# Kernel tuning notes

Measured on AMD Instinct MI355X. Metric: run time of the kernel, lower is better.

The kernel has to match this reference:

```python
import jax, jax.numpy as jnp
import numpy as np

N = 100_000   # num nodes (embedding_shape[0])
E = 1_600_000 # directed edges in adj_t
Q = 500_000   # query edges
D = 256       # embedding_dim == hidden_dim == output_dim


def setup_inputs() -> dict:
    key = jax.random.key(0)
    ks = jax.random.split(key, 12)
    adj_row = jax.random.randint(ks[0], (E,), 0, N, dtype=jnp.int64 if jax.config.jax_enable_x64 else jnp.int32)
    adj_col = jax.random.randint(ks[1], (E,), 0, N, dtype=adj_row.dtype)
    edges = jax.random.randint(ks[2], (2, Q), 0, N, dtype=adj_row.dtype)
    s = 1.0 / np.sqrt(D)
    emb = jax.random.normal(ks[3], (N, D), jnp.float32) * 0.02  # xavier-ish init
    W0 = jax.random.normal(ks[4], (D, D), jnp.float32) * s
    W1 = jax.random.normal(ks[5], (D, D), jnp.float32) * s
    W2 = jax.random.normal(ks[6], (D, D), jnp.float32) * s
    b0 = jnp.zeros((D,), jnp.float32)
    b1 = jnp.zeros((D,), jnp.float32)
    b2 = jnp.zeros((D,), jnp.float32)
    # LinkPredictor: 3 lins (D->D, D->D, D->1)
    P0 = jax.random.normal(ks[7], (D, D), jnp.float32) * s
    P1 = jax.random.normal(ks[8], (D, D), jnp.float32) * s
    P2 = jax.random.normal(ks[9], (D, 1), jnp.float32) * s
    pb0 = jnp.zeros((D,), jnp.float32)
    pb1 = jnp.zeros((D,), jnp.float32)
    pb2 = jnp.zeros((1,), jnp.float32)
    return dict(adj_row=adj_row, adj_col=adj_col, edges=edges, emb=emb,
                W0=W0, b0=b0, W1=W1, b1=b1, W2=W2, b2=b2,
                P0=P0, pb0=pb0, P1=P1, pb1=pb1, P2=P2, pb2=pb2)


def _gcn_norm(adj_row, adj_col):
    # add self loops, symmetric normalization D^-1/2 (A+I) D^-1/2
    loops = jnp.arange(N, dtype=adj_row.dtype)
    row = jnp.concatenate([adj_row, loops])
    col = jnp.concatenate([adj_col, loops])
    deg = jax.ops.segment_sum(jnp.ones(row.shape, jnp.float32), row, num_segments=N)
    dinv = jnp.where(deg > 0, jax.lax.rsqrt(jnp.maximum(deg, 1.0)), 0.0)
    norm = dinv[row] * dinv[col]  # [E+N]
    return row, col, norm


def _gcn_conv(x, W, b, row, col, norm):
    h = x @ W                                   # dense transform [N,D]
    msg = h[col] * norm[:, None]                # gather + scale [E+N,D]
    return jax.ops.segment_sum(msg, row, num_segments=N) + b


def reference(adj_row, adj_col, edges, emb,
              W0, b0, W1, b1, W2, b2,
              P0, pb0, P1, pb1, P2, pb2):
    row, col, norm = _gcn_norm(adj_row, adj_col)
    x = emb
    x = jax.nn.relu(_gcn_conv(x, W0, b0, row, col, norm))  # dropout: no-op (eval)
    x = jax.nn.relu(_gcn_conv(x, W1, b1, row, col, norm))
    x = _gcn_conv(x, W2, b2, row, col, norm)
    # edge-gather + LinkPredictor MLP
    h = x[edges[0]] * x[edges[1]]                # [Q,D]
    h = jax.nn.relu(h @ P0 + pb0)
    h = jax.nn.relu(h @ P1 + pb1)
    out = jax.nn.sigmoid(h @ P2 + pb2)           # [Q,1]
    return out[:, 0]
```

## Files before the change

### kernel.cpp

```cpp
#include <hip/hip_runtime.h>
#include <math.h>

#define D 256

typedef short short8 __attribute__((ext_vector_type(8)));
typedef float f32x4 __attribute__((ext_vector_type(4)));
typedef float f32x2 __attribute__((ext_vector_type(2)));

__device__ __forceinline__ float bf2f(unsigned int h) {
  return __uint_as_float(h << 16);
}
__device__ __forceinline__ unsigned short f2bf(float f) {
  unsigned int u = __float_as_uint(f);
  u += 0x7fffu + ((u >> 16) & 1u);
  return (unsigned short)(u >> 16);
}
__device__ __forceinline__ unsigned int packtrunc(float a, float b) {
  return (__float_as_uint(a) >> 16) | (__float_as_uint(b) & 0xffff0000u);
}
__device__ __forceinline__ unsigned int pk_fp8x4(float a, float b, float c, float d) {
  unsigned int r = 0;
  r = __builtin_amdgcn_cvt_pk_fp8_f32(a, b, r, false);
  r = __builtin_amdgcn_cvt_pk_fp8_f32(c, d, r, true);
  return r;
}
__device__ __forceinline__ void up_fp8x4(unsigned int x, float& a, float& b, float& c,
                                         float& d) {
  f32x2 lo = __builtin_amdgcn_cvt_pk_f32_fp8(x, false);
  f32x2 hi = __builtin_amdgcn_cvt_pk_f32_fp8(x, true);
  a = lo.x; b = lo.y; c = hi.x; d = hi.y;
}

__global__ __launch_bounds__(256) void k_count(const int* __restrict__ row,
                                               int* __restrict__ cnt, int E) {
  int i = blockIdx.x * 256 + threadIdx.x;
  if (i < E) atomicAdd(&cnt[row[i]], 1);
}

__global__ __launch_bounds__(256) void k_scan1(const int* __restrict__ cnt,
                                               int* __restrict__ bsum) {
  __shared__ int sw[4];
  int b = blockIdx.x, tid = threadIdx.x, lane = tid & 63, w = tid >> 6;
  int4 v = *(const int4*)(cnt + (size_t)b * 1024 + tid * 4);
  int s = v.x + v.y + v.z + v.w;
#pragma unroll
  for (int d = 32; d; d >>= 1) s += __shfl_xor(s, d, 64);
  if (lane == 0) sw[w] = s;
  __syncthreads();
  if (tid == 0) bsum[b] = sw[0] + sw[1] + sw[2] + sw[3];
}

__global__ __launch_bounds__(256) void k_scan2(int* __restrict__ bsum, int nb,
                                               int* __restrict__ offs_end) {
  __shared__ int sw[4];
  int tid = threadIdx.x, lane = tid & 63, w = tid >> 6;
  int v = (tid < nb) ? bsum[tid] : 0;
  int x = v;
#pragma unroll
  for (int d = 1; d < 64; d <<= 1) {
    int y = __shfl_up(x, d, 64);
    if (lane >= d) x += y;
  }
  if (lane == 63) sw[w] = x;
  __syncthreads();
  int woff = 0;
  for (int i = 0; i < w; ++i) woff += sw[i];
  int incl = woff + x;
  if (tid < nb) bsum[tid] = incl - v;
  if (tid == 0) *offs_end = sw[0] + sw[1] + sw[2] + sw[3];
}

__global__ __launch_bounds__(256) void k_scan3(const int* __restrict__ cnt,
                                               const int* __restrict__ bbase,
                                               int* __restrict__ offs,
                                               float* __restrict__ dinv) {
  __shared__ int sw[4];
  int b = blockIdx.x, tid = threadIdx.x, lane = tid & 63, w = tid >> 6;
  size_t base = (size_t)b * 1024 + tid * 4;
  int4 v = *(const int4*)(cnt + base);
  int s = v.x + v.y + v.z + v.w;
  int x = s;
#pragma unroll
  for (int d = 1; d < 64; d <<= 1) {
    int y = __shfl_up(x, d, 64);
    if (lane >= d) x += y;
  }
  if (lane == 63) sw[w] = x;
  __syncthreads();
  int woff = bbase[b];
  for (int i = 0; i < w; ++i) woff += sw[i];
  int excl = woff + x - s;
  int4 o;
  o.x = excl;
  o.y = excl + v.x;
  o.z = o.y + v.y;
  o.w = o.z + v.z;
  *(int4*)(offs + base) = o;
  float4 dv;
  dv.x = rsqrtf((float)(v.x + 1));
  dv.y = rsqrtf((float)(v.y + 1));
  dv.z = rsqrtf((float)(v.z + 1));
  dv.w = rsqrtf((float)(v.w + 1));
  *(float4*)(dinv + base) = dv;
}

__global__ __launch_bounds__(256) void k_scatter(const int* __restrict__ row,
                                                 const int* __restrict__ col,
                                                 const int* __restrict__ offs,
                                                 int* __restrict__ cursor,
                                                 const float* __restrict__ dinv,
                                                 int2* __restrict__ csr, int E) {
  int i = blockIdx.x * 256 + threadIdx.x;
  if (i >= E) return;
  int r = row[i];
  int c = col[i];
  int p = atomicAdd(&cursor[r], 1);
  int o = offs[r] + p;
  int2 cn;
  cn.x = c;
  cn.y = __float_as_int(dinv[r] * dinv[c]);
  csr[o] = cn;
}

__global__ __launch_bounds__(256) void k_cast_w(const float* __restrict__ W0,
                                                const float* __restrict__ W1,
                                                const float* __restrict__ W2,
                                                const float* __restrict__ P0,
                                                const float* __restrict__ P1,
                                                unsigned short* __restrict__ Wt) {
  int idx = blockIdx.x * 256 + threadIdx.x;
  int m = idx >> 16;
  int e = idx & 65535;
  int k = e >> 8;
  int n = e & 255;
  const float* src = (m == 0) ? W0 : (m == 1) ? W1 : (m == 2) ? W2 : (m == 3) ? P0 : P1;
  Wt[(size_t)m * 65536 + (size_t)n * D + k] = f2bf(src[(size_t)k * D + n]);
}

__global__ __launch_bounds__(256) void k_cast_emb(const float* __restrict__ emb,
                                                  unsigned short* __restrict__ XA, int N) {
  int idx = blockIdx.x * 256 + threadIdx.x;
  int i = idx >> 6;
  int c4 = (idx & 63) * 4;
  uint2 o;
  o.x = 0u;
  o.y = 0u;
  if (i < N) {
    float4 f = *(const float4*)(emb + (size_t)i * D + c4);
    o.x = (unsigned)f2bf(f.x) | ((unsigned)f2bf(f.y) << 16);
    o.y = (unsigned)f2bf(f.z) | ((unsigned)f2bf(f.w) << 16);
  }
  *(uint2*)(XA + (size_t)i * D + c4) = o;
}

#define TLS 264
__global__ __launch_bounds__(256) void k_gemm(const unsigned short* __restrict__ A,
                                              const unsigned short* __restrict__ Bt,
                                              unsigned int* __restrict__ C8) {
  __shared__ unsigned short tile[64 * TLS];
  int tid = threadIdx.x;
  int lane = tid & 63;
  int w = tid >> 6;
  int quad = lane >> 4;
  int l15 = lane & 15;
  int m0 = blockIdx.x * 64;
  int arow = m0 + w * 16 + l15;
  f32x4 acc[16] = {};
#pragma unroll 2
  for (int k0 = 0; k0 < 256; k0 += 32) {
    short8 a = *(const short8*)(A + (size_t)arow * D + k0 + quad * 8);
#pragma unroll
    for (int t = 0; t < 16; ++t) {
      short8 b = *(const short8*)(Bt + (size_t)(t * 16 + l15) * D + k0 + quad * 8);
      acc[t] = __builtin_amdgcn_mfma_f32_16x16x32_bf16(a, b, acc[t], 0, 0, 0);
    }
  }
  int trow = w * 16 + quad * 4;
#pragma unroll
  for (int t = 0; t < 16; ++t)
#pragma unroll
    for (int r = 0; r < 4; ++r)
      tile[(trow + r) * TLS + t * 16 + l15] = f2bf(acc[t][r]);
  __syncthreads();
  int row = tid >> 2;
  int seg = tid & 3;
  const unsigned short* src = &tile[row * TLS + seg * 64];
  unsigned int* dst = C8 + (((size_t)(m0 + row) * D + seg * 64) >> 2);
#pragma unroll
  for (int k = 0; k < 4; ++k) {
    short8 x0 = *(const short8*)(src + k * 16);
    short8 x1 = *(const short8*)(src + k * 16 + 8);
    uint4 o;
    o.x = pk_fp8x4(bf2f((unsigned short)x0[0]), bf2f((unsigned short)x0[1]),
                   bf2f((unsigned short)x0[2]), bf2f((unsigned short)x0[3]));
    o.y = pk_fp8x4(bf2f((unsigned short)x0[4]), bf2f((unsigned short)x0[5]),
                   bf2f((unsigned short)x0[6]), bf2f((unsigned short)x0[7]));
    o.z = pk_fp8x4(bf2f((unsigned short)x1[0]), bf2f((unsigned short)x1[1]),
                   bf2f((unsigned short)x1[2]), bf2f((unsigned short)x1[3]));
    o.w = pk_fp8x4(bf2f((unsigned short)x1[4]), bf2f((unsigned short)x1[5]),
                   bf2f((unsigned short)x1[6]), bf2f((unsigned short)x1[7]));
    *(uint4*)(dst + k * 4) = o;
  }
}

__global__ __launch_bounds__(256) void k_agg(const unsigned int* __restrict__ h8,
                                             const float* __restrict__ dinv,
                                             const int* __restrict__ offs,
                                             const int2* __restrict__ csr,
                                             const float* __restrict__ bias,
                                             unsigned short* __restrict__ xb,
                                             unsigned int* __restrict__ x8, int mode) {
  int r = blockIdx.x * 4 + (threadIdx.x >> 6);
  int lane = threadIdx.x & 63;
  float dr = dinv[r];
  float wself = dr * dr;
  unsigned int sv = h8[(size_t)r * 64 + lane];
  float a0, a1, a2, a3;
  up_fp8x4(sv, a0, a1, a2, a3);
  a0 *= wself; a1 *= wself; a2 *= wself; a3 *= wself;
  int e0 = offs[r], e1 = offs[r + 1];
  for (int e = e0; e < e1; e += 8) {
    int cc[8];
    float wn[8];
#pragma unroll
    for (int i = 0; i < 8; ++i) {
      bool valid = (e + i) < e1;
      int2 cn = csr[valid ? (e + i) : e0];
      cc[i] = valid ? cn.x : 0;
      wn[i] = valid ? __int_as_float(cn.y) : 0.f;
    }
    unsigned int mm[8];
#pragma unroll
    for (int i = 0; i < 8; ++i) mm[i] = h8[(size_t)cc[i] * 64 + lane];
#pragma unroll
    for (int i = 0; i < 8; ++i) {
      float b0, b1, b2, b3;
      up_fp8x4(mm[i], b0, b1, b2, b3);
      a0 += wn[i] * b0;
      a1 += wn[i] * b1;
      a2 += wn[i] * b2;
      a3 += wn[i] * b3;
    }
  }
  float4 bb = *(const float4*)(bias + lane * 4);
  a0 += bb.x; a1 += bb.y; a2 += bb.z; a3 += bb.w;
  if (mode == 0) {
    a0 = fmaxf(a0, 0.f); a1 = fmaxf(a1, 0.f);
    a2 = fmaxf(a2, 0.f); a3 = fmaxf(a3, 0.f);
    uint2 o;
    o.x = (unsigned)f2bf(a0) | ((unsigned)f2bf(a1) << 16);
    o.y = (unsigned)f2bf(a2) | ((unsigned)f2bf(a3) << 16);
    *(uint2*)(xb + (size_t)r * D + lane * 4) = o;
  } else {
    x8[(size_t)r * 64 + lane] = pk_fp8x4(a0, a1, a2, a3);
  }
}

#define LPS 264
__global__ __launch_bounds__(256, 4) void k_lp(const unsigned char* __restrict__ X8,
                                               const int* __restrict__ eu,
                                               const int* __restrict__ ev,
                                               const unsigned short* __restrict__ P0t,
                                               const float* __restrict__ pb0,
                                               const unsigned short* __restrict__ P1t,
                                               const float* __restrict__ pb1,
                                               const float* __restrict__ P2,
                                               const float* __restrict__ pb2,
                                               float* __restrict__ out, int Q) {
  __shared__ unsigned short hA[64 * LPS];
  __shared__ float sred[4][64];
  int tid = threadIdx.x;
  int lane = tid & 63;
  int w = tid >> 6;
  int quad = lane >> 4;
  int l15 = lane & 15;
  int q0 = blockIdx.x * 64;

  {
    int qi = tid >> 2;
    int seg = tid & 3;
    int q = q0 + qi;
    int u = 0, v = 0;
    if (q < Q) { u = eu[q]; v = ev[q]; }
    const uint4* pu = (const uint4*)(X8 + (size_t)u * 256 + seg * 64);
    const uint4* pv = (const uint4*)(X8 + (size_t)v * 256 + seg * 64);
    uint4 ru[4], rv[4];
#pragma unroll
    for (int c = 0; c < 4; ++c) { ru[c] = pu[c]; rv[c] = pv[c]; }
#pragma unroll
    for (int c = 0; c < 4; ++c) {
      float uf[16], vf[16];
      up_fp8x4(ru[c].x, uf[0], uf[1], uf[2], uf[3]);
      up_fp8x4(ru[c].y, uf[4], uf[5], uf[6], uf[7]);
      up_fp8x4(ru[c].z, uf[8], uf[9], uf[10], uf[11]);
      up_fp8x4(ru[c].w, uf[12], uf[13], uf[14], uf[15]);
      up_fp8x4(rv[c].x, vf[0], vf[1], vf[2], vf[3]);
      up_fp8x4(rv[c].y, vf[4], vf[5], vf[6], vf[7]);
      up_fp8x4(rv[c].z, vf[8], vf[9], vf[10], vf[11]);
      up_fp8x4(rv[c].w, vf[12], vf[13], vf[14], vf[15]);
      uint4 o0, o1;
      if (q < Q) {
        o0.x = packtrunc(uf[0] * vf[0], uf[1] * vf[1]);
        o0.y = packtrunc(uf[2] * vf[2], uf[3] * vf[3]);
        o0.z = packtrunc(uf[4] * vf[4], uf[5] * vf[5]);
        o0.w = packtrunc(uf[6] * vf[6], uf[7] * vf[7]);
        o1.x = packtrunc(uf[8] * vf[8], uf[9] * vf[9]);
        o1.y = packtrunc(uf[10] * vf[10], uf[11] * vf[11]);
        o1.z = packtrunc(uf[12] * vf[12], uf[13] * vf[13]);
        o1.w = packtrunc(uf[14] * vf[14], uf[15] * vf[15]);
      } else {
        o0.x = o0.y = o0.z = o0.w = 0u;
        o1.x = o1.y = o1.z = o1.w = 0u;
      }
      int off = seg * 64 + c * 16;
      *(uint4*)&hA[qi * LPS + off] = o0;
      *(uint4*)&hA[qi * LPS + off + 8] = o1;
    }
  }
  __syncthreads();

  {
    f32x4 acc[4][4] = {};
#pragma unroll
    for (int k0 = 0; k0 < 256; k0 += 32) {
      short8 a[4];
#pragma unroll
      for (int ms = 0; ms < 4; ++ms)
        a[ms] = *(const short8*)&hA[(ms * 16 + l15) * LPS + k0 + quad * 8];
#pragma unroll
      for (int ns = 0; ns < 4; ++ns) {
        short8 b = *(const short8*)(P0t + (size_t)(w * 64 + ns * 16 + l15) * D + k0 + quad * 8);
#pragma unroll
        for (int ms = 0; ms < 4; ++ms)
          acc[ms][ns] = __builtin_amdgcn_mfma_f32_16x16x32_bf16(a[ms], b, acc[ms][ns], 0, 0, 0);
      }
    }
    __syncthreads();
#pragma unroll
    for (int ns = 0; ns < 4; ++ns) {
      int col = w * 64 + ns * 16 + l15;
      float bv = pb0[col];
#pragma unroll
      for (int ms = 0; ms < 4; ++ms) {
        int rbase = ms * 16 + quad * 4;
#pragma unroll
        for (int r = 0; r < 4; ++r) {
          float vv = fmaxf(acc[ms][ns][r] + bv, 0.f);
          hA[(rbase + r) * LPS + col] = f2bf(vv);
        }
      }
    }
    __syncthreads();
  }

  {
    f32x4 acc[4][4] = {};
#pragma unroll
    for (int k0 = 0; k0 < 256; k0 += 32) {
      short8 a[4];
#pragma unroll
      for (int ms = 0; ms < 4; ++ms)
        a[ms] = *(const short8*)&hA[(ms * 16 + l15) * LPS + k0 + quad * 8];
#pragma unroll
      for (int ns = 0; ns < 4; ++ns) {
        short8 b = *(const short8*)(P1t + (size_t)(w * 64 + ns * 16 + l15) * D + k0 + quad * 8);
#pragma unroll
        for (int ms = 0; ms < 4; ++ms)
          acc[ms][ns] = __builtin_amdgcn_mfma_f32_16x16x32_bf16(a[ms], b, acc[ms][ns], 0, 0, 0);
      }
    }
    float p2v[4], pbv[4];
#pragma unroll
    for (int ns = 0; ns < 4; ++ns) {
      int col = w * 64 + ns * 16 + l15;
      p2v[ns] = P2[col];
      pbv[ns] = pb1[col];
    }
    float part[16];
#pragma unroll
    for (int ms = 0; ms < 4; ++ms)
#pragma unroll
      for (int r = 0; r < 4; ++r) {
        float s = 0.f;
#pragma unroll
        for (int ns = 0; ns < 4; ++ns)
          s += fmaxf(acc[ms][ns][r] + pbv[ns], 0.f) * p2v[ns];
        part[ms * 4 + r] = s;
      }
#pragma unroll
    for (int d = 1; d < 16; d <<= 1)
#pragma unroll
      for (int i = 0; i < 16; ++i) part[i] += __shfl_xor(part[i], d, 64);
    if (l15 == 0) {
#pragma unroll
      for (int i = 0; i < 16; ++i) {
        int ms = i >> 2, r = i & 3;
        sred[w][ms * 16 + quad * 4 + r] = part[i];
      }
    }
    __syncthreads();
    if (tid < 64) {
      float s = sred[0][tid] + sred[1][tid] + sred[2][tid] + sred[3][tid] + pb2[0];
      int qq = q0 + tid;
      if (qq < Q) out[qq] = 1.f / (1.f + expf(-s));
    }
  }
}

extern "C" void kernel_launch(void* const* d_in, const int* in_sizes, int n_in,
                              void* d_out, int out_size, void* d_ws, size_t ws_size,
                              hipStream_t stream) {
  const int* adj_row = (const int*)d_in[0];
  const int* adj_col = (const int*)d_in[1];
  const int* edges = (const int*)d_in[2];
  const float* emb = (const float*)d_in[3];
  const float* W0 = (const float*)d_in[4];
  const float* b0 = (const float*)d_in[5];
  const float* W1 = (const float*)d_in[6];
  const float* b1 = (const float*)d_in[7];
  const float* W2 = (const float*)d_in[8];
  const float* b2 = (const float*)d_in[9];
  const float* P0 = (const float*)d_in[10];
  const float* pb0 = (const float*)d_in[11];
  const float* P1 = (const float*)d_in[12];
  const float* pb1 = (const float*)d_in[13];
  const float* P2 = (const float*)d_in[14];
  const float* pb2 = (const float*)d_in[15];
  float* out = (float*)d_out;

  int E = in_sizes[0];
  int Q = in_sizes[2] / 2;
  int N = in_sizes[3] / D;
  int Npad = ((N + 63) / 64) * 64;
  int Npad2 = ((N + 1023) / 1024) * 1024;
  int nb = Npad2 / 1024;

  char* p = (char*)d_ws;
  auto alloc = [&](size_t bytes) {
    char* r = p;
    p += (bytes + 255) & ~(size_t)255;
    return r;
  };
  int* cnt = (int*)alloc((size_t)Npad2 * 4);
  int* cursor = (int*)alloc((size_t)Npad2 * 4);
  int* offs = (int*)alloc((size_t)(Npad2 + 1) * 4);
  float* dinv = (float*)alloc((size_t)Npad2 * 4);
  int* bsum = (int*)alloc((size_t)nb * 4);
  int2* csr = (int2*)alloc((size_t)E * 8);
  unsigned short* Wt = (unsigned short*)alloc((size_t)5 * 65536 * 2);
  unsigned short* XA = (unsigned short*)alloc((size_t)Npad * D * 2);
  unsigned int* XC8 = (unsigned int*)alloc((size_t)Npad * D);
  unsigned int* XA8 = (unsigned int*)XA;

  hipMemsetAsync(cnt, 0, (size_t)Npad2 * 4, stream);
  hipMemsetAsync(cursor, 0, (size_t)Npad2 * 4, stream);

  int eb = (E + 255) / 256;
  k_count<<<eb, 256, 0, stream>>>(adj_row, cnt, E);
  k_scan1<<<nb, 256, 0, stream>>>(cnt, bsum);
  k_scan2<<<1, 256, 0, stream>>>(bsum, nb, offs + Npad2);
  k_scan3<<<nb, 256, 0, stream>>>(cnt, bsum, offs, dinv);
  k_scatter<<<eb, 256, 0, stream>>>(adj_row, adj_col, offs, cursor, dinv, csr, E);
  k_cast_w<<<5 * 65536 / 256, 256, 0, stream>>>(W0, W1, W2, P0, P1, Wt);
  k_cast_emb<<<Npad / 4, 256, 0, stream>>>(emb, XA, N);

  const float* biases[3] = {b0, b1, b2};
  for (int l = 0; l < 3; ++l) {
    k_gemm<<<Npad / 64, 256, 0, stream>>>(XA, Wt + (size_t)l * 65536, XC8);
    k_agg<<<Npad / 4, 256, 0, stream>>>(XC8, dinv, offs, csr, biases[l], XA, XA8,
                                        (l < 2) ? 0 : 1);
  }
  k_lp<<<(Q + 63) / 64, 256, 0, stream>>>((const unsigned char*)XA8, edges, edges + Q,
                                          Wt + (size_t)3 * 65536, pb0,
                                          Wt + (size_t)4 * 65536, pb1, P2, pb2, out, Q);
}
```

Before: 1.196 ms.

## Pipeline gathers in link-predictor and aggregation kernels; tile weight transpose

The link-predictor kernel becomes persistent: each block loops over query tiles and prefetches the next tile's endpoint rows and the index pair two tiles ahead while it runs the MFMA MLP on the current tile. The aggregation kernel double-buffers neighbor gathers, loading the next batch of 8 while accumulating the current one. The weight cast/transpose now goes through a shared-memory tile so reads and writes are coalesced. The cost is higher register pressure: occupancy for k_lp is lowered to 3 blocks, and k_agg holds more live registers.

```diff
diff --git a/kernel.cpp b/kernel.cpp
--- a/kernel.cpp
+++ b/kernel.cpp
@@ -128,13 +128,24 @@
                                                 const float* __restrict__ P0,
                                                 const float* __restrict__ P1,
                                                 unsigned short* __restrict__ Wt) {
-  int idx = blockIdx.x * 256 + threadIdx.x;
-  int m = idx >> 16;
-  int e = idx & 65535;
-  int k = e >> 8;
-  int n = e & 255;
+  __shared__ float tl[32][33];
+  int b = blockIdx.x;
+  int m = b >> 6;
+  int t = b & 63;
+  int tr = (t >> 3) * 32;
+  int tc = (t & 7) * 32;
   const float* src = (m == 0) ? W0 : (m == 1) ? W1 : (m == 2) ? W2 : (m == 3) ? P0 : P1;
-  Wt[(size_t)m * 65536 + (size_t)n * D + k] = f2bf(src[(size_t)k * D + n]);
+  int r = threadIdx.x >> 5, c = threadIdx.x & 31;
+#pragma unroll
+  for (int i = 0; i < 4; ++i)
+    tl[r + i * 8][c] = src[(size_t)(tr + r + i * 8) * D + tc + c];
+  __syncthreads();
+#pragma unroll
+  for (int i = 0; i < 4; ++i) {
+    int n = tc + r + i * 8;
+    int k = tr + c;
+    Wt[(size_t)m * 65536 + (size_t)n * D + k] = f2bf(tl[c][r + i * 8]);
+  }
 }
 
 __global__ __launch_bounds__(256) void k_cast_emb(const float* __restrict__ emb,
@@ -219,27 +230,52 @@
   up_fp8x4(sv, a0, a1, a2, a3);
   a0 *= wself; a1 *= wself; a2 *= wself; a3 *= wself;
   int e0 = offs[r], e1 = offs[r + 1];
+
+  int cc0[8];
+  float wn0[8];
+  unsigned int mm0[8];
+  if (e0 < e1) {
+#pragma unroll
+    for (int i = 0; i < 8; ++i) {
+      bool valid = (e0 + i) < e1;
+      int2 cn = csr[valid ? (e0 + i) : e0];
+      cc0[i] = valid ? cn.x : 0;
+      wn0[i] = valid ? __int_as_float(cn.y) : 0.f;
+    }
+#pragma unroll
+    for (int i = 0; i < 8; ++i) mm0[i] = h8[(size_t)cc0[i] * 64 + lane];
+  }
   for (int e = e0; e < e1; e += 8) {
-    int cc[8];
-    float wn[8];
-#pragma unroll
-    for (int i = 0; i < 8; ++i) {
-      bool valid = (e + i) < e1;
-      int2 cn = csr[valid ? (e + i) : e0];
-      cc[i] = valid ? cn.x : 0;
-      wn[i] = valid ? __int_as_float(cn.y) : 0.f;
-    }
-    unsigned int mm[8];
-#pragma unroll
-    for (int i = 0; i < 8; ++i) mm[i] = h8[(size_t)cc[i] * 64 + lane];
+    int cc1[8];
+    float wn1[8];
+    unsigned int mm1[8];
+    bool nxt = (e + 8) < e1;
+    if (nxt) {
+#pragma unroll
+      for (int i = 0; i < 8; ++i) {
+        bool valid = (e + 8 + i) < e1;
+        int2 cn = csr[valid ? (e + 8 + i) : e0];
+        cc1[i] = valid ? cn.x : 0;
+        wn1[i] = valid ? __int_as_float(cn.y) : 0.f;
+      }
+#pragma unroll
+      for (int i = 0; i < 8; ++i) mm1[i] = h8[(size_t)cc1[i] * 64 + lane];
+    }
 #pragma unroll
     for (int i = 0; i < 8; ++i) {
       float b0, b1, b2, b3;
-      up_fp8x4(mm[i], b0, b1, b2, b3);
-      a0 += wn[i] * b0;
-      a1 += wn[i] * b1;
-      a2 += wn[i] * b2;
-      a3 += wn[i] * b3;
+      up_fp8x4(mm0[i], b0, b1, b2, b3);
+      a0 += wn0[i] * b0;
+      a1 += wn0[i] * b1;
+      a2 += wn0[i] * b2;
+      a3 += wn0[i] * b3;
+    }
+    if (nxt) {
+#pragma unroll
+      for (int i = 0; i < 8; ++i) {
+        mm0[i] = mm1[i];
+        wn0[i] = wn1[i];
+      }
     }
   }
   float4 bb = *(const float4*)(bias + lane * 4);
@@ -257,7 +293,8 @@
 }
 
 #define LPS 264
-__global__ __launch_bounds__(256, 4) void k_lp(const unsigned char* __restrict__ X8,
+#define LP_NB 1536
+__global__ __launch_bounds__(256, 3) void k_lp(const unsigned char* __restrict__ X8,
                                                const int* __restrict__ eu,
                                                const int* __restrict__ ev,
                                                const unsigned short* __restrict__ P0t,
@@ -274,32 +311,47 @@
   int w = tid >> 6;
   int quad = lane >> 4;
   int l15 = lane & 15;
-  int q0 = blockIdx.x * 64;
-
+  int qi = tid >> 2;
+  int seg = tid & 3;
+  int tiles = (Q + 63) >> 6;
+
+  uint4 ru[4], rv[4];
+  int t = blockIdx.x;
   {
-    int qi = tid >> 2;
-    int seg = tid & 3;
-    int q = q0 + qi;
+    int q = t * 64 + qi;
     int u = 0, v = 0;
     if (q < Q) { u = eu[q]; v = ev[q]; }
     const uint4* pu = (const uint4*)(X8 + (size_t)u * 256 + seg * 64);
     const uint4* pv = (const uint4*)(X8 + (size_t)v * 256 + seg * 64);
-    uint4 ru[4], rv[4];
 #pragma unroll
     for (int c = 0; c < 4; ++c) { ru[c] = pu[c]; rv[c] = pv[c]; }
-#pragma unroll
-    for (int c = 0; c < 4; ++c) {
-      float uf[16], vf[16];
-      up_fp8x4(ru[c].x, uf[0], uf[1], uf[2], uf[3]);
-      up_fp8x4(ru[c].y, uf[4], uf[5], uf[6], uf[7]);
-      up_fp8x4(ru[c].z, uf[8], uf[9], uf[10], uf[11]);
-      up_fp8x4(ru[c].w, uf[12], uf[13], uf[14], uf[15]);
-      up_fp8x4(rv[c].x, vf[0], vf[1], vf[2], vf[3]);
-      up_fp8x4(rv[c].y, vf[4], vf[5], vf[6], vf[7]);
-      up_fp8x4(rv[c].z, vf[8], vf[9], vf[10], vf[11]);
-      up_fp8x4(rv[c].w, vf[12], vf[13], vf[14], vf[15]);
-      uint4 o0, o1;
-      if (q < Q) {
+  }
+  int uB = 0, vB = 0;
+  {
+    int q = (t + LP_NB) * 64 + qi;
+    if (q < Q) { uB = eu[q]; vB = ev[q]; }
+  }
+
+  for (; t < tiles; t += LP_NB) {
+    int uC = 0, vC = 0;
+    {
+      int q = (t + 2 * LP_NB) * 64 + qi;
+      if (q < Q) { uC = eu[q]; vC = ev[q]; }
+    }
+    __syncthreads();
+    {
+#pragma unroll
+      for (int c = 0; c < 4; ++c) {
+        float uf[16], vf[16];
+        up_fp8x4(ru[c].x, uf[0], uf[1], uf[2], uf[3]);
+        up_fp8x4(ru[c].y, uf[4], uf[5], uf[6], uf[7]);
+        up_fp8x4(ru[c].z, uf[8], uf[9], uf[10], uf[11]);
+        up_fp8x4(ru[c].w, uf[12], uf[13], uf[14], uf[15]);
+        up_fp8x4(rv[c].x, vf[0], vf[1], vf[2], vf[3]);
+        up_fp8x4(rv[c].y, vf[4], vf[5], vf[6], vf[7]);
+        up_fp8x4(rv[c].z, vf[8], vf[9], vf[10], vf[11]);
+        up_fp8x4(rv[c].w, vf[12], vf[13], vf[14], vf[15]);
+        uint4 o0, o1;
         o0.x = packtrunc(uf[0] * vf[0], uf[1] * vf[1]);
         o0.y = packtrunc(uf[2] * vf[2], uf[3] * vf[3]);
         o0.z = packtrunc(uf[4] * vf[4], uf[5] * vf[5]);
@@ -308,102 +360,107 @@
         o1.y = packtrunc(uf[10] * vf[10], uf[11] * vf[11]);
         o1.z = packtrunc(uf[12] * vf[12], uf[13] * vf[13]);
         o1.w = packtrunc(uf[14] * vf[14], uf[15] * vf[15]);
-      } else {
-        o0.x = o0.y = o0.z = o0.w = 0u;
-        o1.x = o1.y = o1.z = o1.w = 0u;
-      }
-      int off = seg * 64 + c * 16;
-      *(uint4*)&hA[qi * LPS + off] = o0;
-      *(uint4*)&hA[qi * LPS + off + 8] = o1;
-    }
-  }
-  __syncthreads();
-
-  {
-    f32x4 acc[4][4] = {};
-#pragma unroll
-    for (int k0 = 0; k0 < 256; k0 += 32) {
-      short8 a[4];
+        int off = seg * 64 + c * 16;
+        *(uint4*)&hA[qi * LPS + off] = o0;
+        *(uint4*)&hA[qi * LPS + off + 8] = o1;
+      }
+    }
+    if (t + LP_NB < tiles) {
+      const uint4* pu = (const uint4*)(X8 + (size_t)uB * 256 + seg * 64);
+      const uint4* pv = (const uint4*)(X8 + (size_t)vB * 256 + seg * 64);
+#pragma unroll
+      for (int c = 0; c < 4; ++c) { ru[c] = pu[c]; rv[c] = pv[c]; }
+    }
+    __syncthreads();
+
+    {
+      f32x4 acc[4][4] = {};
+#pragma unroll
+      for (int k0 = 0; k0 < 256; k0 += 32) {
+        short8 a[4];
+#pragma unroll
+        for (int ms = 0; ms < 4; ++ms)
+          a[ms] = *(const short8*)&hA[(ms * 16 + l15) * LPS + k0 + quad * 8];
+#pragma unroll
+        for (int ns = 0; ns < 4; ++ns) {
+          short8 b = *(const short8*)(P0t + (size_t)(w * 64 + ns * 16 + l15) * D + k0 + quad * 8);
+#pragma unroll
+          for (int ms = 0; ms < 4; ++ms)
+            acc[ms][ns] = __builtin_amdgcn_mfma_f32_16x16x32_bf16(a[ms], b, acc[ms][ns], 0, 0, 0);
+        }
+      }
+      __syncthreads();
+#pragma unroll
+      for (int ns = 0; ns < 4; ++ns) {
+        int col = w * 64 + ns * 16 + l15;
+        float bv = pb0[col];
+#pragma unroll
+        for (int ms = 0; ms < 4; ++ms) {
+          int rbase = ms * 16 + quad * 4;
+#pragma unroll
+          for (int r = 0; r < 4; ++r) {
+            float vv = fmaxf(acc[ms][ns][r] + bv, 0.f);
+            hA[(rbase + r) * LPS + col] = f2bf(vv);
+          }
+        }
+      }
+      __syncthreads();
+    }
+
+    {
+      f32x4 acc[4][4] = {};
+#pragma unroll
+      for (int k0 = 0; k0 < 256; k0 += 32) {
+        short8 a[4];
+#pragma unroll
+        for (int ms = 0; ms < 4; ++ms)
+          a[ms] = *(const short8*)&hA[(ms * 16 + l15) * LPS + k0 + quad * 8];
+#pragma unroll
+        for (int ns = 0; ns < 4; ++ns) {
+          short8 b = *(const short8*)(P1t + (size_t)(w * 64 + ns * 16 + l15) * D + k0 + quad * 8);
+#pragma unroll
+          for (int ms = 0; ms < 4; ++ms)
+            acc[ms][ns] = __builtin_amdgcn_mfma_f32_16x16x32_bf16(a[ms], b, acc[ms][ns], 0, 0, 0);
+        }
+      }
+      float p2v[4], pbv[4];
+#pragma unroll
+      for (int ns = 0; ns < 4; ++ns) {
+        int col = w * 64 + ns * 16 + l15;
+        p2v[ns] = P2[col];
+        pbv[ns] = pb1[col];
+      }
+      float part[16];
 #pragma unroll
       for (int ms = 0; ms < 4; ++ms)
-        a[ms] = *(const short8*)&hA[(ms * 16 + l15) * LPS + k0 + quad * 8];
-#pragma unroll
-      for (int ns = 0; ns < 4; ++ns) {
-        short8 b = *(const short8*)(P0t + (size_t)(w * 64 + ns * 16 + l15) * D + k0 + quad * 8);
-#pragma unroll
-        for (int ms = 0; ms < 4; ++ms)
-          acc[ms][ns] = __builtin_amdgcn_mfma_f32_16x16x32_bf16(a[ms], b, acc[ms][ns], 0, 0, 0);
-      }
-    }
-    __syncthreads();
-#pragma unroll
-    for (int ns = 0; ns < 4; ++ns) {
-      int col = w * 64 + ns * 16 + l15;
-      float bv = pb0[col];
-#pragma unroll
-      for (int ms = 0; ms < 4; ++ms) {
-        int rbase = ms * 16 + quad * 4;
 #pragma unroll
         for (int r = 0; r < 4; ++r) {
-          float vv = fmaxf(acc[ms][ns][r] + bv, 0.f);
-          hA[(rbase + r) * LPS + col] = f2bf(vv);
+          float s = 0.f;
+#pragma unroll
+          for (int ns = 0; ns < 4; ++ns)
+            s += fmaxf(acc[ms][ns][r] + pbv[ns], 0.f) * p2v[ns];
+          part[ms * 4 + r] = s;
         }
-      }
-    }
-    __syncthreads();
-  }
-
-  {
-    f32x4 acc[4][4] = {};
-#pragma unroll
-    for (int k0 = 0; k0 < 256; k0 += 32) {
-      short8 a[4];
-#pragma unroll
-      for (int ms = 0; ms < 4; ++ms)
-        a[ms] = *(const short8*)&hA[(ms * 16 + l15) * LPS + k0 + quad * 8];
-#pragma unroll
-      for (int ns = 0; ns < 4; ++ns) {
-        short8 b = *(const short8*)(P1t + (size_t)(w * 64 + ns * 16 + l15) * D + k0 + quad * 8);
-#pragma unroll
-        for (int ms = 0; ms < 4; ++ms)
-          acc[ms][ns] = __builtin_amdgcn_mfma_f32_16x16x32_bf16(a[ms], b, acc[ms][ns], 0, 0, 0);
-      }
-    }
-    float p2v[4], pbv[4];
-#pragma unroll
-    for (int ns = 0; ns < 4; ++ns) {
-      int col = w * 64 + ns * 16 + l15;
-      p2v[ns] = P2[col];
-      pbv[ns] = pb1[col];
-    }
-    float part[16];
-#pragma unroll
-    for (int ms = 0; ms < 4; ++ms)
-#pragma unroll
-      for (int r = 0; r < 4; ++r) {
-        float s = 0.f;
-#pragma unroll
-        for (int ns = 0; ns < 4; ++ns)
-          s += fmaxf(acc[ms][ns][r] + pbv[ns], 0.f) * p2v[ns];
-        part[ms * 4 + r] = s;
-      }
-#pragma unroll
-    for (int d = 1; d < 16; d <<= 1)
-#pragma unroll
-      for (int i = 0; i < 16; ++i) part[i] += __shfl_xor(part[i], d, 64);
-    if (l15 == 0) {
-#pragma unroll
-      for (int i = 0; i < 16; ++i) {
-        int ms = i >> 2, r = i & 3;
-        sred[w][ms * 16 + quad * 4 + r] = part[i];
-      }
-    }
-    __syncthreads();
-    if (tid < 64) {
-      float s = sred[0][tid] + sred[1][tid] + sred[2][tid] + sred[3][tid] + pb2[0];
-      int qq = q0 + tid;
-      if (qq < Q) out[qq] = 1.f / (1.f + expf(-s));
-    }
+#pragma unroll
+      for (int d = 1; d < 16; d <<= 1)
+#pragma unroll
+        for (int i = 0; i < 16; ++i) part[i] += __shfl_xor(part[i], d, 64);
+      if (l15 == 0) {
+#pragma unroll
+        for (int i = 0; i < 16; ++i) {
+          int ms = i >> 2, r = i & 3;
+          sred[w][ms * 16 + quad * 4 + r] = part[i];
+        }
+      }
+      __syncthreads();
+      if (tid < 64) {
+        float s = sred[0][tid] + sred[1][tid] + sred[2][tid] + sred[3][tid] + pb2[0];
+        int qq = t * 64 + tid;
+        if (qq < Q) out[qq] = 1.f / (1.f + expf(-s));
+      }
+    }
+    uB = uC;
+    vB = vC;
   }
 }
 
@@ -461,7 +518,7 @@
   k_scan2<<<1, 256, 0, stream>>>(bsum, nb, offs + Npad2);
   k_scan3<<<nb, 256, 0, stream>>>(cnt, bsum, offs, dinv);
   k_scatter<<<eb, 256, 0, stream>>>(adj_row, adj_col, offs, cursor, dinv, csr, E);
-  k_cast_w<<<5 * 65536 / 256, 256, 0, stream>>>(W0, W1, W2, P0, P1, Wt);
+  k_cast_w<<<5 * 64, 256, 0, stream>>>(W0, W1, W2, P0, P1, Wt);
   k_cast_emb<<<Npad / 4, 256, 0, stream>>>(emb, XA, N);
 
   const float* biases[3] = {b0, b1, b2};
@@ -470,7 +527,7 @@
     k_agg<<<Npad / 4, 256, 0, stream>>>(XC8, dinv, offs, csr, biases[l], XA, XA8,
                                         (l < 2) ? 0 : 1);
   }
-  k_lp<<<(Q + 63) / 64, 256, 0, stream>>>((const unsigned char*)XA8, edges, edges + Q,
-                                          Wt + (size_t)3 * 65536, pb0,
-                                          Wt + (size_t)4 * 65536, pb1, P2, pb2, out, Q);
-}
+  k_lp<<<LP_NB, 256, 0, stream>>>((const unsigned char*)XA8, edges, edges + Q,
+                                  Wt + (size_t)3 * 65536, pb0,
+                                  Wt + (size_t)4 * 65536, pb1, P2, pb2, out, Q);
+}
```

Result: slower. 1.416 ms (+18.4%).

## Restructure GCN aggregation to 16 lanes per row with pipelined gathers

Applied to the files above, without the earlier changes.

The aggregation kernel now assigns 16 lanes per destination row (4 rows per wavefront) so each lane loads 16 fp8 values with a 128-bit load instead of 4 bytes. Neighbor gathers are software-pipelined with a depth-4 prefetch of the next batch of CSR entries and feature rows, which keeps more memory requests in flight. Weight transposition now goes through a shared-memory 32x32 tile so both reads and writes are coalesced. The cost is higher register pressure from 16 accumulators plus double-buffered uint4 loads, and the prefetch issues redundant loads of row 0 for padded slots.

```diff
diff --git a/kernel.cpp b/kernel.cpp
--- a/kernel.cpp
+++ b/kernel.cpp
@@ -128,13 +128,24 @@
                                                 const float* __restrict__ P0,
                                                 const float* __restrict__ P1,
                                                 unsigned short* __restrict__ Wt) {
-  int idx = blockIdx.x * 256 + threadIdx.x;
-  int m = idx >> 16;
-  int e = idx & 65535;
-  int k = e >> 8;
-  int n = e & 255;
+  __shared__ float tl[32][33];
+  int b = blockIdx.x;
+  int m = b >> 6;
+  int t = b & 63;
+  int tr = (t >> 3) * 32;
+  int tc = (t & 7) * 32;
   const float* src = (m == 0) ? W0 : (m == 1) ? W1 : (m == 2) ? W2 : (m == 3) ? P0 : P1;
-  Wt[(size_t)m * 65536 + (size_t)n * D + k] = f2bf(src[(size_t)k * D + n]);
+  int r = threadIdx.x >> 5, c = threadIdx.x & 31;
+#pragma unroll
+  for (int i = 0; i < 4; ++i)
+    tl[r + i * 8][c] = src[(size_t)(tr + r + i * 8) * D + tc + c];
+  __syncthreads();
+#pragma unroll
+  for (int i = 0; i < 4; ++i) {
+    int n = tc + r + i * 8;
+    int k = tr + c;
+    Wt[(size_t)m * 65536 + (size_t)n * D + k] = f2bf(tl[c][r + i * 8]);
+  }
 }
 
 __global__ __launch_bounds__(256) void k_cast_emb(const float* __restrict__ emb,
@@ -203,56 +214,107 @@
   }
 }
 
-__global__ __launch_bounds__(256) void k_agg(const unsigned int* __restrict__ h8,
+__global__ __launch_bounds__(256) void k_agg(const unsigned char* __restrict__ X8,
                                              const float* __restrict__ dinv,
                                              const int* __restrict__ offs,
                                              const int2* __restrict__ csr,
                                              const float* __restrict__ bias,
                                              unsigned short* __restrict__ xb,
                                              unsigned int* __restrict__ x8, int mode) {
-  int r = blockIdx.x * 4 + (threadIdx.x >> 6);
-  int lane = threadIdx.x & 63;
+  int tid = threadIdx.x;
+  int w = tid >> 6;
+  int lane = tid & 63;
+  int s = lane >> 4;
+  int l15 = lane & 15;
+  int r = blockIdx.x * 16 + w * 4 + s;
   float dr = dinv[r];
   float wself = dr * dr;
-  unsigned int sv = h8[(size_t)r * 64 + lane];
-  float a0, a1, a2, a3;
-  up_fp8x4(sv, a0, a1, a2, a3);
-  a0 *= wself; a1 *= wself; a2 *= wself; a3 *= wself;
-  int e0 = offs[r], e1 = offs[r + 1];
-  for (int e = e0; e < e1; e += 8) {
-    int cc[8];
-    float wn[8];
-#pragma unroll
-    for (int i = 0; i < 8; ++i) {
-      bool valid = (e + i) < e1;
-      int2 cn = csr[valid ? (e + i) : e0];
-      cc[i] = valid ? cn.x : 0;
-      wn[i] = valid ? __int_as_float(cn.y) : 0.f;
-    }
-    unsigned int mm[8];
-#pragma unroll
-    for (int i = 0; i < 8; ++i) mm[i] = h8[(size_t)cc[i] * 64 + lane];
-#pragma unroll
-    for (int i = 0; i < 8; ++i) {
-      float b0, b1, b2, b3;
-      up_fp8x4(mm[i], b0, b1, b2, b3);
-      a0 += wn[i] * b0;
-      a1 += wn[i] * b1;
-      a2 += wn[i] * b2;
-      a3 += wn[i] * b3;
-    }
-  }
-  float4 bb = *(const float4*)(bias + lane * 4);
-  a0 += bb.x; a1 += bb.y; a2 += bb.z; a3 += bb.w;
+  int es = offs[r], en = offs[r + 1];
+
+  float acc[16];
+  {
+    uint4 sv = *(const uint4*)(X8 + (size_t)r * 256 + l15 * 16);
+    float f[16];
+    up_fp8x4(sv.x, f[0], f[1], f[2], f[3]);
+    up_fp8x4(sv.y, f[4], f[5], f[6], f[7]);
+    up_fp8x4(sv.z, f[8], f[9], f[10], f[11]);
+    up_fp8x4(sv.w, f[12], f[13], f[14], f[15]);
+#pragma unroll
+    for (int k = 0; k < 16; ++k) acc[k] = wself * f[k];
+  }
+
+  const int DEPTH = 4;
+  float wns[DEPTH];
+  uint4 mm[DEPTH];
+#pragma unroll
+  for (int j = 0; j < DEPTH; ++j) {
+    bool v = (es + j) < en;
+    int idx = v ? (es + j) : 0;
+    int2 cn = csr[idx];
+    int col = v ? cn.x : 0;
+    wns[j] = v ? __int_as_float(cn.y) : 0.f;
+    mm[j] = *(const uint4*)(X8 + (size_t)col * 256 + l15 * 16);
+  }
+
+  for (int e = es; e < en; e += DEPTH) {
+    float nwns[DEPTH];
+    uint4 nmm[DEPTH];
+#pragma unroll
+    for (int j = 0; j < DEPTH; ++j) {
+      bool v = (e + DEPTH + j) < en;
+      int idx = v ? (e + DEPTH + j) : 0;
+      int2 cn = csr[idx];
+      int col = v ? cn.x : 0;
+      nwns[j] = v ? __int_as_float(cn.y) : 0.f;
+      nmm[j] = *(const uint4*)(X8 + (size_t)col * 256 + l15 * 16);
+    }
+#pragma unroll
+    for (int j = 0; j < DEPTH; ++j) {
+      float f[16];
+      up_fp8x4(mm[j].x, f[0], f[1], f[2], f[3]);
+      up_fp8x4(mm[j].y, f[4], f[5], f[6], f[7]);
+      up_fp8x4(mm[j].z, f[8], f[9], f[10], f[11]);
+      up_fp8x4(mm[j].w, f[12], f[13], f[14], f[15]);
+#pragma unroll
+      for (int k = 0; k < 16; ++k) acc[k] += wns[j] * f[k];
+    }
+#pragma unroll
+    for (int j = 0; j < DEPTH; ++j) {
+      mm[j] = nmm[j];
+      wns[j] = nwns[j];
+    }
+  }
+
+#pragma unroll
+  for (int k = 0; k < 4; ++k) {
+    float4 bb = *(const float4*)(bias + l15 * 16 + k * 4);
+    acc[k * 4 + 0] += bb.x;
+    acc[k * 4 + 1] += bb.y;
+    acc[k * 4 + 2] += bb.z;
+    acc[k * 4 + 3] += bb.w;
+  }
   if (mode == 0) {
-    a0 = fmaxf(a0, 0.f); a1 = fmaxf(a1, 0.f);
-    a2 = fmaxf(a2, 0.f); a3 = fmaxf(a3, 0.f);
-    uint2 o;
-    o.x = (unsigned)f2bf(a0) | ((unsigned)f2bf(a1) << 16);
-    o.y = (unsigned)f2bf(a2) | ((unsigned)f2bf(a3) << 16);
-    *(uint2*)(xb + (size_t)r * D + lane * 4) = o;
+#pragma unroll
+    for (int k = 0; k < 16; ++k) acc[k] = fmaxf(acc[k], 0.f);
+    uint4 o0, o1;
+    o0.x = (unsigned)f2bf(acc[0]) | ((unsigned)f2bf(acc[1]) << 16);
+    o0.y = (unsigned)f2bf(acc[2]) | ((unsigned)f2bf(acc[3]) << 16);
+    o0.z = (unsigned)f2bf(acc[4]) | ((unsigned)f2bf(acc[5]) << 16);
+    o0.w = (unsigned)f2bf(acc[6]) | ((unsigned)f2bf(acc[7]) << 16);
+    o1.x = (unsigned)f2bf(acc[8]) | ((unsigned)f2bf(acc[9]) << 16);
+    o1.y = (unsigned)f2bf(acc[10]) | ((unsigned)f2bf(acc[11]) << 16);
+    o1.z = (unsigned)f2bf(acc[12]) | ((unsigned)f2bf(acc[13]) << 16);
+    o1.w = (unsigned)f2bf(acc[14]) | ((unsigned)f2bf(acc[15]) << 16);
+    unsigned short* dst = xb + (size_t)r * D + l15 * 16;
+    *(uint4*)dst = o0;
+    *(uint4*)(dst + 8) = o1;
   } else {
-    x8[(size_t)r * 64 + lane] = pk_fp8x4(a0, a1, a2, a3);
+    uint4 o;
+    o.x = pk_fp8x4(acc[0], acc[1], acc[2], acc[3]);
+    o.y = pk_fp8x4(acc[4], acc[5], acc[6], acc[7]);
+    o.z = pk_fp8x4(acc[8], acc[9], acc[10], acc[11]);
+    o.w = pk_fp8x4(acc[12], acc[13], acc[14], acc[15]);
+    *(uint4*)(x8 + (size_t)r * 64 + l15 * 4) = o;
   }
 }
 
@@ -461,14 +523,14 @@
   k_scan2<<<1, 256, 0, stream>>>(bsum, nb, offs + Npad2);
   k_scan3<<<nb, 256, 0, stream>>>(cnt, bsum, offs, dinv);
   k_scatter<<<eb, 256, 0, stream>>>(adj_row, adj_col, offs, cursor, dinv, csr, E);
-  k_cast_w<<<5 * 65536 / 256, 256, 0, stream>>>(W0, W1, W2, P0, P1, Wt);
+  k_cast_w<<<5 * 64, 256, 0, stream>>>(W0, W1, W2, P0, P1, Wt);
   k_cast_emb<<<Npad / 4, 256, 0, stream>>>(emb, XA, N);
 
   const float* biases[3] = {b0, b1, b2};
   for (int l = 0; l < 3; ++l) {
     k_gemm<<<Npad / 64, 256, 0, stream>>>(XA, Wt + (size_t)l * 65536, XC8);
-    k_agg<<<Npad / 4, 256, 0, stream>>>(XC8, dinv, offs, csr, biases[l], XA, XA8,
-                                        (l < 2) ? 0 : 1);
+    k_agg<<<Npad / 16, 256, 0, stream>>>((const unsigned char*)XC8, dinv, offs, csr,
+                                         biases[l], XA, XA8, (l < 2) ? 0 : 1);
   }
   k_lp<<<(Q + 63) / 64, 256, 0, stream>>>((const unsigned char*)XA8, edges, edges + Q,
                                           Wt + (size_t)3 * 65536, pb0,
```

Result: no change. 1.210 ms (+1.1%).
